# Kernel optimization log

Hardware: AMD Instinct MI355X
Metric: run time of the kernel (lower is better)

Reference implementation:

```python
import jax, jax.numpy as jnp
import numpy as np


def setup_inputs() -> dict:
    key = jax.random.key(0)
    ks = jax.random.split(key, 9)
    B, LAT, OBS, HID = 4096, 128, 64, 1024
    s = 0.05  # keep tanh out of full saturation
    return {
        "z": jax.random.normal(ks[0], (B, LAT), jnp.float32),
        "W_l2h": jax.random.normal(ks[1], (HID, LAT), jnp.float32) * s,
        "b_l2h": jax.random.normal(ks[2], (HID,), jnp.float32) * s,
        "W_ih": jax.random.normal(ks[3], (HID, OBS), jnp.float32) * s,
        "b_ih": jax.random.normal(ks[4], (HID,), jnp.float32) * s,
        "W_hh": jax.random.normal(ks[5], (HID, HID), jnp.float32) * s,
        "b_hh": jax.random.normal(ks[6], (HID,), jnp.float32) * s,
        "W_ho": jax.random.normal(ks[7], (OBS, HID), jnp.float32) * s,
        "b_ho": jax.random.normal(ks[8], (OBS,), jnp.float32) * s,
        "seq_len": 70,
    }


def reference(z, W_l2h, b_l2h, W_ih, b_ih, W_hh, b_hh, W_ho, b_ho, seq_len):
    B = z.shape[0]
    obs_dim = W_ho.shape[0]
    # latent -> initial hidden state (nn.Linear)
    h0 = z @ W_l2h.T + b_l2h                         # [B, HID]
    x0 = jnp.zeros((B, obs_dim), dtype=z.dtype)      # first RNN input is zeros

    def step(carry, _):
        h, x = carry
        # tanh RNN cell: h' = tanh(x W_ih^T + b_ih + h W_hh^T + b_hh)
        h = jnp.tanh(x @ W_ih.T + b_ih + h @ W_hh.T + b_hh)
        y = h @ W_ho.T + b_ho                        # output projection [B, OBS]
        x_next = jax.lax.stop_gradient(y)
        return (h, x_next), y

    _, ys = jax.lax.scan(step, (h0, x0), None, length=seq_len)  # [T, B, OBS]
    return jnp.transpose(ys, (1, 0, 2))              # [B, T, OBS]
```

## Files before the change

kernel.cpp:

```cpp
#include <hip/hip_runtime.h>
#include <hip/hip_bf16.h>
#include <stdint.h>

typedef _Float16 f16;
typedef _Float16 f16x8 __attribute__((ext_vector_type(8)));
typedef float f32x4 __attribute__((ext_vector_type(4)));

#define B_SZ 4096
#define HID  1024
#define LAT  128
#define OBS  64
#define TSEQ 70
#define SPLIT_SCALE 2048.0f
#define SPLIT_INV   (1.0f / 2048.0f)

__device__ __forceinline__ size_t tidx(int row, int k, int K) {
  return (size_t)((row >> 4) * (K >> 5) + (k >> 5)) * 512
       + ((k >> 3) & 3) * 128 + (row & 15) * 8 + (k & 7);
}

__device__ __forceinline__ void gl2lds16(const void* g, void* l) {
  __builtin_amdgcn_global_load_lds(
      (const __attribute__((address_space(1))) void*)g,
      (__attribute__((address_space(3))) void*)l, 16, 0, 0);
}

__device__ __forceinline__ float tanh_fast(float x) {
  float e = __expf(2.0f * x);
  return 1.0f - 2.0f / (e + 1.0f);
}

__global__ __launch_bounds__(256, 2) void rnn_step_split(
    const f16* __restrict__ Ah, const f16* __restrict__ Al,
    const f16* __restrict__ Wh, const f16* __restrict__ Wl,
    const float* __restrict__ bias,
    f16* __restrict__ Hh, f16* __restrict__ Hl, int K)
{
  __shared__ __align__(16) f16 ring[3][24 * 512];

  const int lane = threadIdx.x & 63;
  const int wave = threadIdx.x >> 6;
  const int bm = blockIdx.x;
  const int bn = blockIdx.y;
  const int lo8 = lane * 8;
  const int kc = K >> 5;

  f32x4 acc0[2][4], acc1[2][4];
  const f32x4 z4 = {0.f, 0.f, 0.f, 0.f};
#pragma unroll
  for (int i = 0; i < 2; ++i)
#pragma unroll
    for (int j = 0; j < 4; ++j) { acc0[i][j] = z4; acc1[i][j] = z4; }

  auto stage = [&](int it, int slot) {
    f16* b = ring[slot];
#pragma unroll
    for (int u = 0; u < 2; ++u) {
      const int rg = wave * 2 + u;
      const size_t ga = (size_t)((bm * 8 + rg) * kc + it) * 512 + lo8;
      gl2lds16(Ah + ga, b + rg * 512);
      gl2lds16(Al + ga, b + (8 + rg) * 512);
    }
    const size_t gw = (size_t)((bn * 4 + wave) * kc + it) * 512 + lo8;
    gl2lds16(Wh + gw, b + (16 + wave) * 512);
    gl2lds16(Wl + gw, b + (20 + wave) * 512);
  };

  auto compute = [&](int slot) {
    const f16* b = ring[slot];
    f16x8 vah[2], val[2], vwh[4], vwl[4];
#pragma unroll
    for (int i = 0; i < 2; ++i) {
      vah[i] = *(const f16x8*)&b[(wave * 2 + i) * 512 + lo8];
      val[i] = *(const f16x8*)&b[(8 + wave * 2 + i) * 512 + lo8];
    }
#pragma unroll
    for (int j = 0; j < 4; ++j) {
      vwh[j] = *(const f16x8*)&b[(16 + j) * 512 + lo8];
      vwl[j] = *(const f16x8*)&b[(20 + j) * 512 + lo8];
    }
#pragma unroll
    for (int i = 0; i < 2; ++i)
#pragma unroll
      for (int j = 0; j < 4; ++j) {
        acc0[i][j] = __builtin_amdgcn_mfma_f32_16x16x32_f16(vah[i], vwh[j], acc0[i][j], 0, 0, 0);
        acc1[i][j] = __builtin_amdgcn_mfma_f32_16x16x32_f16(vah[i], vwl[j], acc1[i][j], 0, 0, 0);
        acc1[i][j] = __builtin_amdgcn_mfma_f32_16x16x32_f16(val[i], vwh[j], acc1[i][j], 0, 0, 0);
      }
  };

  stage(0, 0);
  int cur = 0;
  for (int it = 0; it + 1 < kc; ++it) {
    const int nxt = (cur == 2) ? 0 : cur + 1;
    stage(it + 1, nxt);
    asm volatile("s_waitcnt vmcnt(6)" ::: "memory");
    __builtin_amdgcn_s_barrier();
    compute(cur);
    cur = nxt;
  }
  asm volatile("s_waitcnt vmcnt(0)" ::: "memory");
  __builtin_amdgcn_s_barrier();
  compute(cur);

  const int rq = lane >> 4;
  const int cl = lane & 15;
#pragma unroll
  for (int j = 0; j < 4; ++j) {
    const int gcol = bn * 64 + j * 16 + cl;
    const float bb = bias[gcol];
#pragma unroll
    for (int i = 0; i < 2; ++i) {
      const int grow = bm * 128 + wave * 32 + i * 16 + rq * 4;
#pragma unroll
      for (int r = 0; r < 4; ++r) {
        const float a = acc0[i][j][r] + acc1[i][j][r] * SPLIT_INV + bb;
        const float t = tanh_fast(a);
        const f16 hi = (f16)t;
        const size_t idx = tidx(grow + r, gcol, HID);
        Hh[idx] = hi;
        Hl[idx] = (f16)((t - (float)hi) * SPLIT_SCALE);
      }
    }
  }
}

__global__ __launch_bounds__(256, 2) void proj_kernel(
    const f16* __restrict__ H, const f16* __restrict__ Who,
    const float* __restrict__ bho, float* __restrict__ Y, int t0)
{
  __shared__ __align__(16) f16 As[128 * 64];
  __shared__ __align__(16) f16 Bs[64 * 64];
  const int lane = threadIdx.x & 63;
  const int wave = threadIdx.x >> 6;
  const int bm = blockIdx.x;
  const int lo8 = lane * 8;

  f32x4 acc[2][4];
  const f32x4 z4 = {0.f, 0.f, 0.f, 0.f};
#pragma unroll
  for (int i = 0; i < 2; ++i)
#pragma unroll
    for (int j = 0; j < 4; ++j) acc[i][j] = z4;

  for (int kt = 0; kt < HID; kt += 64) {
    const int kch = kt >> 5;
#pragma unroll
    for (int u = 0; u < 4; ++u) {
      const int cidx = wave * 4 + u;
      const int mt = cidx >> 1, s = cidx & 1;
      gl2lds16(H + (size_t)((bm * 8 + mt) * 32 + kch + s) * 512 + lo8, &As[cidx * 512]);
    }
#pragma unroll
    for (int u = 0; u < 2; ++u) {
      const int cidx = wave * 2 + u;
      const int nt = cidx >> 1, s = cidx & 1;
      gl2lds16(Who + (size_t)(nt * 32 + kch + s) * 512 + lo8, &Bs[cidx * 512]);
    }
    __syncthreads();
#pragma unroll
    for (int s = 0; s < 2; ++s) {
      f16x8 af[2], bfr[4];
#pragma unroll
      for (int i = 0; i < 2; ++i)
        af[i] = *(const f16x8*)&As[(((wave * 2 + i) << 1) | s) * 512 + lo8];
#pragma unroll
      for (int j = 0; j < 4; ++j)
        bfr[j] = *(const f16x8*)&Bs[((j << 1) | s) * 512 + lo8];
#pragma unroll
      for (int i = 0; i < 2; ++i)
#pragma unroll
        for (int j = 0; j < 4; ++j)
          acc[i][j] = __builtin_amdgcn_mfma_f32_16x16x32_f16(af[i], bfr[j], acc[i][j], 0, 0, 0);
    }
    __syncthreads();
  }

  const int rq = lane >> 4;
  const int cl = lane & 15;
#pragma unroll
  for (int j = 0; j < 4; ++j) {
    const int col = j * 16 + cl;
    const float bb = bho[col];
#pragma unroll
    for (int i = 0; i < 2; ++i)
#pragma unroll
      for (int r = 0; r < 4; ++r) {
        const int row = bm * 128 + wave * 32 + i * 16 + rq * 4 + r;
        const int t = t0 + (row >> 12);
        const int b = row & 4095;
        Y[((size_t)b * TSEQ + t) * OBS + col] = acc[i][j][r] + bb;
      }
  }
}

__global__ void cast_tiled_kernel(const float* __restrict__ x, f16* __restrict__ y,
                                  int K, int n) {
  int i = blockIdx.x * blockDim.x + threadIdx.x;
  if (i < n) y[tidx(i / K, i % K, K)] = (f16)x[i];
}

__global__ void split_tiled_kernel(const float* __restrict__ x, f16* __restrict__ hi,
                                   f16* __restrict__ lo, int K, int n) {
  int i = blockIdx.x * blockDim.x + threadIdx.x;
  if (i < n) {
    float v = x[i];
    f16 h = (f16)v;
    size_t o = tidx(i / K, i % K, K);
    hi[o] = h;
    lo[o] = (f16)((v - (float)h) * SPLIT_SCALE);
  }
}

__global__ void prep_weff(const float* __restrict__ Whh, const float* __restrict__ Wih,
                          const float* __restrict__ Who,
                          f16* __restrict__ Wh, f16* __restrict__ Wl) {
  const int n = blockIdx.x;
  __shared__ float wih_row[OBS];
  if (threadIdx.x < OBS) wih_row[threadIdx.x] = Wih[n * OBS + threadIdx.x];
  __syncthreads();
  for (int k = threadIdx.x; k < HID; k += 256) {
    float s = Whh[(size_t)n * HID + k];
#pragma unroll 8
    for (int o = 0; o < OBS; ++o) s = fmaf(wih_row[o], Who[(size_t)o * HID + k], s);
    const size_t idx = tidx(n, k, HID);
    f16 h = (f16)s;
    Wh[idx] = h;
    Wl[idx] = (f16)((s - (float)h) * SPLIT_SCALE);
  }
}

__global__ void prep_w1(const float* __restrict__ Whh, const float* __restrict__ Wl2h,
                        f16* __restrict__ W1h, f16* __restrict__ W1l) {
  const int n = blockIdx.x, j = threadIdx.x;
  float s = 0.f;
  for (int k = 0; k < HID; ++k) s = fmaf(Whh[(size_t)n * HID + k], Wl2h[(size_t)k * LAT + j], s);
  const size_t idx = tidx(n, j, LAT);
  f16 h = (f16)s;
  W1h[idx] = h;
  W1l[idx] = (f16)((s - (float)h) * SPLIT_SCALE);
}

__global__ void prep_bias(const float* __restrict__ bih, const float* __restrict__ bhh,
                          const float* __restrict__ bho, const float* __restrict__ Wih,
                          const float* __restrict__ Whh, const float* __restrict__ bl2h,
                          float* __restrict__ beff, float* __restrict__ b1) {
  const int n = blockIdx.x, l = threadIdx.x;
  float s1 = Wih[(size_t)n * OBS + l] * bho[l];
  float s2 = 0.f;
  for (int k = l; k < HID; k += 64) s2 = fmaf(Whh[(size_t)n * HID + k], bl2h[k], s2);
#pragma unroll
  for (int off = 32; off > 0; off >>= 1) {
    s1 += __shfl_down(s1, off);
    s2 += __shfl_down(s2, off);
  }
  if (l == 0) {
    const float base = bih[n] + bhh[n];
    beff[n] = base + s1;
    b1[n]   = base + s2;
  }
}

extern "C" void kernel_launch(void* const* d_in, const int* in_sizes, int n_in,
                              void* d_out, int out_size, void* d_ws, size_t ws_size,
                              hipStream_t stream) {
  (void)in_sizes; (void)n_in; (void)out_size; (void)ws_size;
  const float* z    = (const float*)d_in[0];
  const float* Wl2h = (const float*)d_in[1];
  const float* bl2h = (const float*)d_in[2];
  const float* Wih  = (const float*)d_in[3];
  const float* bih  = (const float*)d_in[4];
  const float* Whh  = (const float*)d_in[5];
  const float* bhh  = (const float*)d_in[6];
  const float* Who  = (const float*)d_in[7];
  const float* bho  = (const float*)d_in[8];
  float* Y = (float*)d_out;

  char* ws = (char*)d_ws;
  size_t off = 0;
  auto take = [&](size_t bytes) {
    char* p = ws + off;
    off = (off + bytes + 255) & ~(size_t)255;
    return p;
  };
  f16*   Weffh = (f16*)take((size_t)HID * HID * 2);
  f16*   Weffl = (f16*)take((size_t)HID * HID * 2);
  f16*   W1h   = (f16*)take((size_t)HID * LAT * 2);
  f16*   W1l   = (f16*)take((size_t)HID * LAT * 2);
  f16*   Whob  = (f16*)take((size_t)OBS * HID * 2);
  f16*   zh    = (f16*)take((size_t)B_SZ * LAT * 2);
  f16*   zl    = (f16*)take((size_t)B_SZ * LAT * 2);
  float* beff  = (float*)take(HID * 4);
  float* b1    = (float*)take(HID * 4);

  const size_t S = (size_t)B_SZ * HID;
  f16* Hlo  = (f16*)take(2 * S * 2);
  f16* ring = (f16*)take(8 * S * 2);

  split_tiled_kernel<<<(B_SZ * LAT) / 256, 256, 0, stream>>>(z, zh, zl, LAT, B_SZ * LAT);
  cast_tiled_kernel<<<(OBS * HID) / 256, 256, 0, stream>>>(Who, Whob, HID, OBS * HID);
  prep_weff<<<HID, 256, 0, stream>>>(Whh, Wih, Who, Weffh, Weffl);
  prep_w1<<<HID, LAT, 0, stream>>>(Whh, Wl2h, W1h, W1l);
  prep_bias<<<HID, 64, 0, stream>>>(bih, bhh, bho, Wih, Whh, bl2h, beff, b1);

  dim3 sgrid(B_SZ / 128, HID / 64);
  rnn_step_split<<<sgrid, 256, 0, stream>>>(zh, zl, W1h, W1l, b1, ring, Hlo, LAT);
  for (int t = 1; t < TSEQ; ++t) {
    if ((t & 7) == 0)
      proj_kernel<<<(8 * B_SZ) / 128, 256, 0, stream>>>(ring, Whob, bho, Y, t - 8);
    rnn_step_split<<<sgrid, 256, 0, stream>>>(
        ring + (size_t)((t - 1) & 7) * S, Hlo + (size_t)((t - 1) & 1) * S,
        Weffh, Weffl, beff,
        ring + (size_t)(t & 7) * S, Hlo + (size_t)(t & 1) * S, HID);
  }
  proj_kernel<<<(6 * B_SZ) / 128, 256, 0, stream>>>(ring, Whob, bho, Y, 64);
}
```

Measured before the change: 2.180 ms.

## Widen RNN step tile to 128x128 with 8 waves and dynamic LDS

Changes the recurrent step kernel from 256 threads computing a 128x64 output tile to 512 threads (8 waves as 4x2) computing a 128x128 tile, with a 3-slot dynamic LDS ring of 32KB slots. Each A tile loaded from global is now reused across twice as many output columns, halving the redundant hidden-state reads across the N grid. It raises LDS use to 96KB per block, which with launch bounds of 2 may limit occupancy to one block per CU, and halves the grid size.

```diff
diff --git a/kernel.cpp b/kernel.cpp
--- a/kernel.cpp
+++ b/kernel.cpp
@@ -30,16 +30,19 @@
   return 1.0f - 2.0f / (e + 1.0f);
 }
 
-__global__ __launch_bounds__(256, 2) void rnn_step_split(
+__global__ __launch_bounds__(512, 2) void rnn_step_split(
     const f16* __restrict__ Ah, const f16* __restrict__ Al,
     const f16* __restrict__ Wh, const f16* __restrict__ Wl,
     const float* __restrict__ bias,
     f16* __restrict__ Hh, f16* __restrict__ Hl, int K)
 {
-  __shared__ __align__(16) f16 ring[3][24 * 512];
+  extern __shared__ __align__(16) f16 lds[];
+  const int SLOT = 32 * 512;
 
   const int lane = threadIdx.x & 63;
   const int wave = threadIdx.x >> 6;
+  const int mrow = wave & 3;
+  const int ncol = wave >> 2;
   const int bm = blockIdx.x;
   const int bn = blockIdx.y;
   const int lo8 = lane * 8;
@@ -53,31 +56,27 @@
     for (int j = 0; j < 4; ++j) { acc0[i][j] = z4; acc1[i][j] = z4; }
 
   auto stage = [&](int it, int slot) {
-    f16* b = ring[slot];
-#pragma unroll
-    for (int u = 0; u < 2; ++u) {
-      const int rg = wave * 2 + u;
-      const size_t ga = (size_t)((bm * 8 + rg) * kc + it) * 512 + lo8;
-      gl2lds16(Ah + ga, b + rg * 512);
-      gl2lds16(Al + ga, b + (8 + rg) * 512);
-    }
-    const size_t gw = (size_t)((bn * 4 + wave) * kc + it) * 512 + lo8;
+    f16* b = lds + slot * SLOT;
+    const size_t ga = (size_t)((bm * 8 + wave) * kc + it) * 512 + lo8;
+    gl2lds16(Ah + ga, b + wave * 512);
+    gl2lds16(Al + ga, b + (8 + wave) * 512);
+    const size_t gw = (size_t)((bn * 8 + wave) * kc + it) * 512 + lo8;
     gl2lds16(Wh + gw, b + (16 + wave) * 512);
-    gl2lds16(Wl + gw, b + (20 + wave) * 512);
+    gl2lds16(Wl + gw, b + (24 + wave) * 512);
   };
 
   auto compute = [&](int slot) {
-    const f16* b = ring[slot];
+    const f16* b = lds + slot * SLOT;
     f16x8 vah[2], val[2], vwh[4], vwl[4];
 #pragma unroll
     for (int i = 0; i < 2; ++i) {
-      vah[i] = *(const f16x8*)&b[(wave * 2 + i) * 512 + lo8];
-      val[i] = *(const f16x8*)&b[(8 + wave * 2 + i) * 512 + lo8];
+      vah[i] = *(const f16x8*)&b[(mrow * 2 + i) * 512 + lo8];
+      val[i] = *(const f16x8*)&b[(8 + mrow * 2 + i) * 512 + lo8];
     }
 #pragma unroll
     for (int j = 0; j < 4; ++j) {
-      vwh[j] = *(const f16x8*)&b[(16 + j) * 512 + lo8];
-      vwl[j] = *(const f16x8*)&b[(20 + j) * 512 + lo8];
+      vwh[j] = *(const f16x8*)&b[(16 + ncol * 4 + j) * 512 + lo8];
+      vwl[j] = *(const f16x8*)&b[(24 + ncol * 4 + j) * 512 + lo8];
     }
 #pragma unroll
     for (int i = 0; i < 2; ++i)
@@ -94,7 +93,7 @@
   for (int it = 0; it + 1 < kc; ++it) {
     const int nxt = (cur == 2) ? 0 : cur + 1;
     stage(it + 1, nxt);
-    asm volatile("s_waitcnt vmcnt(6)" ::: "memory");
+    asm volatile("s_waitcnt vmcnt(4)" ::: "memory");
     __builtin_amdgcn_s_barrier();
     compute(cur);
     cur = nxt;
@@ -107,11 +106,11 @@
   const int cl = lane & 15;
 #pragma unroll
   for (int j = 0; j < 4; ++j) {
-    const int gcol = bn * 64 + j * 16 + cl;
+    const int gcol = bn * 128 + ncol * 64 + j * 16 + cl;
     const float bb = bias[gcol];
 #pragma unroll
     for (int i = 0; i < 2; ++i) {
-      const int grow = bm * 128 + wave * 32 + i * 16 + rq * 4;
+      const int grow = bm * 128 + mrow * 32 + i * 16 + rq * 4;
 #pragma unroll
       for (int r = 0; r < 4; ++r) {
         const float a = acc0[i][j][r] + acc1[i][j][r] * SPLIT_INV + bb;
@@ -275,6 +274,13 @@
   const float* Who  = (const float*)d_in[7];
   const float* bho  = (const float*)d_in[8];
   float* Y = (float*)d_out;
+
+  static bool configured = false;
+  if (!configured) {
+    hipFuncSetAttribute(reinterpret_cast<const void*>(rnn_step_split),
+                        hipFuncAttributeMaxDynamicSharedMemorySize, 98304);
+    configured = true;
+  }
 
   char* ws = (char*)d_ws;
   size_t off = 0;
@@ -303,12 +309,12 @@
   prep_w1<<<HID, LAT, 0, stream>>>(Whh, Wl2h, W1h, W1l);
   prep_bias<<<HID, 64, 0, stream>>>(bih, bhh, bho, Wih, Whh, bl2h, beff, b1);
 
-  dim3 sgrid(B_SZ / 128, HID / 64);
-  rnn_step_split<<<sgrid, 256, 0, stream>>>(zh, zl, W1h, W1l, b1, ring, Hlo, LAT);
+  dim3 sgrid(B_SZ / 128, HID / 128);
+  rnn_step_split<<<sgrid, 512, 98304, stream>>>(zh, zl, W1h, W1l, b1, ring, Hlo, LAT);
   for (int t = 1; t < TSEQ; ++t) {
     if ((t & 7) == 0)
       proj_kernel<<<(8 * B_SZ) / 128, 256, 0, stream>>>(ring, Whob, bho, Y, t - 8);
-    rnn_step_split<<<sgrid, 256, 0, stream>>>(
+    rnn_step_split<<<sgrid, 512, 98304, stream>>>(
         ring + (size_t)((t - 1) & 7) * S, Hlo + (size_t)((t - 1) & 1) * S,
         Weffh, Weffl, beff,
         ring + (size_t)(t & 7) * S, Hlo + (size_t)(t & 1) * S, HID);
```

After: 2.344 ms. 1.08x slower.
